# Optimization experiments

Hardware: AMD Instinct MI355X
Metric: run time of the kernel (lower is better)

## Reference

```python
import jax, jax.numpy as jnp
import numpy as np

B, S, D = 1, 2048, 2048
H = 16
HD = D // H           # 128
FFN_H = 5632          # int(2*4*D/3) rounded up to multiple of 256
EPS = 1e-5
ROPE_THETA = 10000.0


def rms_norm(x, w, eps=EPS):
    # x * rsqrt(mean(x^2, -1) + eps) * w
    return x * jax.lax.rsqrt(jnp.mean(x * x, axis=-1, keepdims=True) + eps) * w


def apply_rope(x, cos, sin):
    # x: [B, S, H, HD]; cos/sin: [S, HD//2]
    b, s, h, hd = x.shape
    xr = x.reshape(b, s, h, hd // 2, 2)
    x_re, x_im = xr[..., 0], xr[..., 1]
    c = cos[None, :, None, :]
    sn = sin[None, :, None, :]
    o_re = x_re * c - x_im * sn
    o_im = x_re * sn + x_im * c
    return jnp.stack([o_re, o_im], axis=-1).reshape(b, s, h, hd)


def setup_inputs() -> dict:
    key = jax.random.key(0)
    ks = jax.random.split(key, 10)
    x = jax.random.normal(ks[0], (B, S, D), dtype=jnp.float32)
    # RoPE frequencies (Llama-style)
    inv_freq = 1.0 / (ROPE_THETA ** (np.arange(0, HD, 2, dtype=np.float32) / HD))
    angles = np.outer(np.arange(S, dtype=np.float32), inv_freq)  # [S, HD//2]
    freqs_cos = jnp.asarray(np.cos(angles), dtype=jnp.float32)
    freqs_sin = jnp.asarray(np.sin(angles), dtype=jnp.float32)
    # causal mask: 1 = keep, 0 = masked
    mask = jnp.tril(jnp.ones((S, S), dtype=jnp.int32))[None, None]
    sc = 0.02
    return {
        "x": x,
        "freqs_cos": freqs_cos,
        "freqs_sin": freqs_sin,
        "mask": mask,
        "wq": jax.random.normal(ks[1], (D, D), jnp.float32) * sc,
        "wk": jax.random.normal(ks[2], (D, D), jnp.float32) * sc,
        "wv": jax.random.normal(ks[3], (D, D), jnp.float32) * sc,
        "wo": jax.random.normal(ks[4], (D, D), jnp.float32) * sc,
        "w1": jax.random.normal(ks[5], (D, FFN_H), jnp.float32) * sc,
        "w2": jax.random.normal(ks[6], (FFN_H, D), jnp.float32) * sc,
        "w3": jax.random.normal(ks[7], (D, FFN_H), jnp.float32) * sc,
        "attn_norm_w": jnp.ones((D,), jnp.float32),
        "ffn_norm_w": jnp.ones((D,), jnp.float32),
    }


def reference(x, freqs_cos, freqs_sin, mask, wq, wk, wv, wo, w1, w2, w3,
              attn_norm_w, ffn_norm_w):
    b, s, d = x.shape
    # --- attention block ---
    xn = rms_norm(x, attn_norm_w)
    q = (xn @ wq).reshape(b, s, H, HD)
    k = (xn @ wk).reshape(b, s, H, HD)
    v = (xn @ wv).reshape(b, s, H, HD)
    q = apply_rope(q, freqs_cos, freqs_sin)
    k = apply_rope(k, freqs_cos, freqs_sin)
    scores = jnp.einsum('bqhd,bkhd->bhqk', q, k) / jnp.sqrt(jnp.float32(HD))
    scores = jnp.where(mask == 0, -jnp.inf, scores)
    probs = jax.nn.softmax(scores, axis=-1)
    attn = jnp.einsum('bhqk,bkhd->bqhd', probs, v).reshape(b, s, d)
    h = x + attn @ wo
    # --- SwiGLU FFN block ---
    hn = rms_norm(h, ffn_norm_w)
    ff = (jax.nn.silu(hn @ w1) * (hn @ w3)) @ w2
    return h + ff
```

## Files before the change

kernel.cpp:

```cpp
#include <hip/hip_runtime.h>
#include <hip/hip_bf16.h>

typedef __bf16 bf16x8 __attribute__((ext_vector_type(8)));
typedef float f32x4 __attribute__((ext_vector_type(4)));
typedef unsigned short u16x8 __attribute__((ext_vector_type(8)));
typedef unsigned short u16x4 __attribute__((ext_vector_type(4)));

#define DEV static __device__ __forceinline__

DEV unsigned short f2bf(float f) {
    unsigned u = __builtin_bit_cast(unsigned, f);
    u += 0x7fffu + ((u >> 16) & 1u);
    return (unsigned short)(u >> 16);
}
DEV float bf2f(unsigned short h) {
    unsigned u = ((unsigned)h) << 16;
    return __builtin_bit_cast(float, u);
}

DEV void gl2lds16(const void* g, void* l) {
    __builtin_amdgcn_global_load_lds(
        (const __attribute__((address_space(1))) void*)g,
        (__attribute__((address_space(3))) void*)l, 16, 0, 0);
}

#define WAITV(N) asm volatile("s_waitcnt vmcnt(" #N ")" ::: "memory")
#define SBAR()   asm volatile("s_barrier" ::: "memory")

#define STAGE128D(KT, BUF)                                                    \
    _Pragma("unroll")                                                         \
    for (int sl = 0; sl < 3; ++sl) {                                          \
        const unsigned short* sbase = (sl == 0)                               \
            ? A  + (size_t)bm * K                                             \
            : BT + (size_t)(bn + (sl - 1) * 128) * K;                         \
        _Pragma("unroll")                                                     \
        for (int j = 0; j < 2; ++j) {                                         \
            const unsigned short* g = sbase + (size_t)(srow + j * 64) * K     \
                                      + koff + (KT) * 64 + lc;                \
            gl2lds16(g, &lds[BUF][sl][wave * 512 + j * 4096]);                \
        }                                                                     \
    }

#define DSREAD128(BUF)                                                        \
    {                                                                         \
        const char* Ab = (const char*)&lds[BUF][0][0];                        \
        const char* Bb = (const char*)&lds[BUF][1 + (wn >> 1)][0];            \
        _Pragma("unroll")                                                     \
        for (int m4 = 0; m4 < 4; ++m4)                                        \
            _Pragma("unroll")                                                 \
            for (int kk = 0; kk < 2; ++kk)                                    \
                a_[m4][kk] = *(const bf16x8*)(Ab +                            \
                    (wm * 64 + m4 * 16 + lr) * 128 +                          \
                    ((kk * 64 + lg * 16) ^ xsw));                             \
        _Pragma("unroll")                                                     \
        for (int n2 = 0; n2 < 4; ++n2)                                        \
            _Pragma("unroll")                                                 \
            for (int kk = 0; kk < 2; ++kk)                                    \
                b_[n2][kk] = *(const bf16x8*)(Bb +                            \
                    ((wn & 1) * 64 + n2 * 16 + lr) * 128 +                    \
                    ((kk * 64 + lg * 16) ^ xsw));                             \
    }

#define MFMA128                                                               \
    __builtin_amdgcn_s_setprio(1);                                            \
    _Pragma("unroll")                                                         \
    for (int m4 = 0; m4 < 4; ++m4)                                            \
        _Pragma("unroll")                                                     \
        for (int n2 = 0; n2 < 4; ++n2)                                        \
            _Pragma("unroll")                                                 \
            for (int kk = 0; kk < 2; ++kk)                                    \
                acc[m4][n2] = __builtin_amdgcn_mfma_f32_16x16x32_bf16(        \
                    a_[m4][kk], b_[n2][kk], acc[m4][n2], 0, 0, 0);            \
    __builtin_amdgcn_s_setprio(0);

template <int EPI>
__global__ __launch_bounds__(512, 2)
void gemm128d(const unsigned short* __restrict__ A,
              const unsigned short* __restrict__ BT,
              unsigned short* __restrict__ outB,
              float* __restrict__ outP,
              int M, int N, int K)
{
    __shared__ alignas(16) unsigned short lds[3][3][8192];
    const int tid  = threadIdx.x;
    const int lane = tid & 63;
    const int wave = tid >> 6;
    const int wm = wave >> 2;
    const int wn = wave & 3;
    const int lr = lane & 15;
    const int lg = lane >> 4;
    const int gy  = gridDim.y;
    const int lin = blockIdx.y * gridDim.x + blockIdx.x;
    const int cpx = (gridDim.x * gy) >> 3;
    const int swz = (lin & 7) * cpx + (lin >> 3);
    const int bm = (swz % gy) * 128;
    const int bn = (swz / gy) * 256;
    const int xsw  = (lr & 7) << 4;
    const int srow = tid >> 3;
    const int lc   = ((tid & 7) ^ (srow & 7)) * 8;
    int koff, NT;
    if constexpr (EPI == 1) { const int Kh = K >> 1; koff = blockIdx.z * Kh; NT = Kh >> 6; }
    else                    { koff = 0;              NT = K >> 6; }

    f32x4 acc[4][4] = {};
    bf16x8 a_[4][2], b_[4][2];

    STAGE128D(0, 0);
    STAGE128D(1, 1);
    WAITV(6); SBAR();
    DSREAD128(0);

    int bc = 0;
    for (int kt = 0; kt < NT - 2; ++kt) {
        const int nb = (bc == 0) ? 2 : bc - 1;
        STAGE128D(kt + 2, nb);
        MFMA128;
        WAITV(6); SBAR();
        const int rb = (bc == 2) ? 0 : bc + 1;
        DSREAD128(rb);
        bc = rb;
    }
    MFMA128;
    WAITV(0); SBAR();
    {
        const int rb = (bc == 2) ? 0 : bc + 1;
        DSREAD128(rb);
    }
    MFMA128;

#pragma unroll
    for (int m4 = 0; m4 < 4; ++m4) {
        const int row = bm + wm * 64 + m4 * 16 + lg * 4;
#pragma unroll
        for (int n2 = 0; n2 < 4; ++n2) {
            const int col = bn + wn * 64 + n2 * 16 + lr;
#pragma unroll
            for (int r = 0; r < 4; ++r) {
                if constexpr (EPI == 0) {
                    outB[(size_t)(row + r) * N + col] = f2bf(acc[m4][n2][r]);
                } else if constexpr (EPI == 1) {
                    outP[(size_t)blockIdx.z * M * N + (size_t)(row + r) * N + col] = acc[m4][n2][r];
                } else {
                    const float v  = acc[m4][n2][r];
                    const float vo = __shfl_xor(v, 1);
                    const float x1 = (lr & 1) ? vo : v;
                    const float x3 = (lr & 1) ? v : vo;
                    const float g  = x1 / (1.0f + __expf(-x1)) * x3;
                    if (!(lr & 1))
                        outB[(size_t)(row + r) * (N >> 1) + (col >> 1)] = f2bf(g);
                }
            }
        }
    }
}

__global__ __launch_bounds__(256)
void reduce2_add(const float* res, const float* p, float* out, int n4)
{
    const float4* r4 = (const float4*)res;
    const float4* a4 = (const float4*)p;
    const float4* b4 = (const float4*)(p + (size_t)2048 * 2048);
    float4* o4 = (float4*)out;
    for (int i = blockIdx.x * 256 + threadIdx.x; i < n4; i += gridDim.x * 256) {
        const float4 r = r4[i], a = a4[i], b = b4[i];
        o4[i] = make_float4(r.x + a.x + b.x, r.y + a.y + b.y,
                            r.z + a.z + b.z, r.w + a.w + b.w);
    }
}

__global__ __launch_bounds__(256)
void reduce2_norm(const float* __restrict__ res, const float* __restrict__ p,
                  const float* __restrict__ w, float* __restrict__ hout,
                  unsigned short* __restrict__ nout)
{
    const int row = blockIdx.x, tid = threadIdx.x;
    const float4* r4 = (const float4*)(res + (size_t)row * 2048);
    const float4* a4 = (const float4*)(p   + (size_t)row * 2048);
    const float4* b4 = (const float4*)(p + (size_t)2048 * 2048 + (size_t)row * 2048);
    float4* h4 = (float4*)(hout + (size_t)row * 2048);
    float4 h[2];
    float ss = 0.f;
#pragma unroll
    for (int i = 0; i < 2; ++i) {
        const int idx = i * 256 + tid;
        const float4 r = r4[idx], a = a4[idx], b = b4[idx];
        float4 v = make_float4(r.x + a.x + b.x, r.y + a.y + b.y,
                               r.z + a.z + b.z, r.w + a.w + b.w);
        h[i] = v; h4[idx] = v;
        ss += v.x * v.x + v.y * v.y + v.z * v.z + v.w * v.w;
    }
#pragma unroll
    for (int off = 32; off; off >>= 1) ss += __shfl_xor(ss, off);
    __shared__ float red[4];
    if ((tid & 63) == 0) red[tid >> 6] = ss;
    __syncthreads();
    const float tot = red[0] + red[1] + red[2] + red[3];
    const float sc = rsqrtf(tot * (1.0f / 2048.0f) + 1e-5f);
#pragma unroll
    for (int i = 0; i < 2; ++i) {
        const int idx = i * 256 + tid;
        const float4 wv = ((const float4*)w)[idx];
        u16x4 o;
        o[0] = f2bf(h[i].x * sc * wv.x); o[1] = f2bf(h[i].y * sc * wv.y);
        o[2] = f2bf(h[i].z * sc * wv.z); o[3] = f2bf(h[i].w * sc * wv.w);
        *(u16x4*)(nout + (size_t)row * 2048 + idx * 4) = o;
    }
}

__global__ __launch_bounds__(256)
void rmsnorm_kernel(const float* __restrict__ x, const float* __restrict__ w,
                    unsigned short* __restrict__ out)
{
    const int row = blockIdx.x;
    const int tid = threadIdx.x;
    const float* xr = x + (size_t)row * 2048;
    const float4 a = *reinterpret_cast<const float4*>(xr + tid * 8);
    const float4 b = *reinterpret_cast<const float4*>(xr + tid * 8 + 4);
    float ss = a.x * a.x + a.y * a.y + a.z * a.z + a.w * a.w
             + b.x * b.x + b.y * b.y + b.z * b.z + b.w * b.w;
#pragma unroll
    for (int off = 32; off; off >>= 1) ss += __shfl_xor(ss, off);
    __shared__ float red[4];
    if ((tid & 63) == 0) red[tid >> 6] = ss;
    __syncthreads();
    const float tot = red[0] + red[1] + red[2] + red[3];
    const float sc = rsqrtf(tot * (1.0f / 2048.0f) + 1e-5f);
    const float4 wa = *reinterpret_cast<const float4*>(w + tid * 8);
    const float4 wb = *reinterpret_cast<const float4*>(w + tid * 8 + 4);
    u16x8 o;
    o[0] = f2bf(a.x * sc * wa.x); o[1] = f2bf(a.y * sc * wa.y);
    o[2] = f2bf(a.z * sc * wa.z); o[3] = f2bf(a.w * sc * wa.w);
    o[4] = f2bf(b.x * sc * wb.x); o[5] = f2bf(b.y * sc * wb.y);
    o[6] = f2bf(b.z * sc * wb.z); o[7] = f2bf(b.w * sc * wb.w);
    *reinterpret_cast<u16x8*>(out + (size_t)row * 2048 + tid * 8) = o;
}

__global__ __launch_bounds__(256)
void rope_kernel(unsigned short* __restrict__ t, const float* __restrict__ cs,
                 const float* __restrict__ sn)
{
    const int idx = blockIdx.x * 256 + threadIdx.x;
    const int s   = idx >> 9;
    const int col = (idx & 511) * 8;
    const int i0  = (col & 127) >> 1;
    u16x8 v = *reinterpret_cast<const u16x8*>(t + (size_t)s * 6144 + col);
    const float4 c  = *reinterpret_cast<const float4*>(cs + s * 64 + i0);
    const float4 sv = *reinterpret_cast<const float4*>(sn + s * 64 + i0);
    const float cc[4] = {c.x, c.y, c.z, c.w};
    const float ns[4] = {sv.x, sv.y, sv.z, sv.w};
#pragma unroll
    for (int p = 0; p < 4; ++p) {
        const float re = bf2f(v[2 * p]), im = bf2f(v[2 * p + 1]);
        v[2 * p]     = f2bf(re * cc[p] - im * ns[p]);
        v[2 * p + 1] = f2bf(re * ns[p] + im * cc[p]);
    }
    *reinterpret_cast<u16x8*>(t + (size_t)s * 6144 + col) = v;
}

__global__ __launch_bounds__(256)
void transpose_bf16(const unsigned short* __restrict__ in,
                    unsigned short* __restrict__ out, int M, int N, int ldin)
{
    __shared__ unsigned short t[64][66];
    const int bm = blockIdx.y * 64, bn = blockIdx.x * 64;
    const int tid = threadIdx.x;
    const int r = tid >> 3, c8 = (tid & 7) * 8;
#pragma unroll
    for (int i = 0; i < 2; ++i) {
        const int row = r + i * 32;
        u16x8 v = *reinterpret_cast<const u16x8*>(in + (size_t)(bm + row) * ldin + bn + c8);
#pragma unroll
        for (int e = 0; e < 8; ++e) t[row][c8 + e] = v[e];
    }
    __syncthreads();
#pragma unroll
    for (int i = 0; i < 2; ++i) {
        const int orow = r + i * 32;
        u16x8 v;
#pragma unroll
        for (int e = 0; e < 8; ++e) v[e] = t[c8 + e][orow];
        *reinterpret_cast<u16x8*>(out + (size_t)(bn + orow) * M + bm + c8) = v;
    }
}

__global__ __launch_bounds__(256)
void convT_kernel(const float* __restrict__ w, unsigned short* __restrict__ wT,
                  int K, int N, int rmul, int radd)
{
    __shared__ unsigned short t[64][66];
    const int bk = blockIdx.y * 64, bn = blockIdx.x * 64;
    const int tid = threadIdx.x;
    const int r = tid >> 4, c4 = (tid & 15) * 4;
#pragma unroll
    for (int i = 0; i < 4; ++i) {
        const int row = r + i * 16;
        const float4 v = *reinterpret_cast<const float4*>(w + (size_t)(bk + row) * N + bn + c4);
        t[row][c4 + 0] = f2bf(v.x); t[row][c4 + 1] = f2bf(v.y);
        t[row][c4 + 2] = f2bf(v.z); t[row][c4 + 3] = f2bf(v.w);
    }
    __syncthreads();
#pragma unroll
    for (int i = 0; i < 4; ++i) {
        const int n = r + i * 16;
        u16x4 o;
#pragma unroll
        for (int e = 0; e < 4; ++e) o[e] = t[c4 + e][n];
        *reinterpret_cast<u16x4*>(wT + (size_t)(rmul * (bn + n) + radd) * K + bk + c4) = o;
    }
}

__global__ __launch_bounds__(512)
void flash_attn(const unsigned short* __restrict__ q,
                const unsigned short* __restrict__ k,
                const unsigned short* __restrict__ vT,
                unsigned short* __restrict__ attn)
{
    __shared__ alignas(16) unsigned short Ks[2][64][136];
    __shared__ alignas(16) unsigned short Vs[2][128][72];
    __shared__ alignas(16) unsigned short Ps[8][16][72];

    const int hh = blockIdx.y;
    const int pi = blockIdx.x;
    const int tid = threadIdx.x;
    const int lane = tid & 63, wave = tid >> 6;
    const int qt = (wave >> 2) ? (31 - pi) : pi;
    const int lr = lane & 15, lg = lane >> 4;
    const int q0 = qt * 64 + (wave & 3) * 16;
    const int myNT = qt + 1;
    const int NT   = 32 - pi;

    const int kr0 = tid >> 4, kc0 = (tid & 15) * 8;
    const int vr0 = tid >> 3, vc0 = (tid & 7) * 8;

    bf16x8 qf[4];
#pragma unroll
    for (int c = 0; c < 4; ++c)
        qf[c] = *reinterpret_cast<const bf16x8*>(
            q + (size_t)(q0 + lr) * 6144 + hh * 128 + c * 32 + lg * 8);

    f32x4 oacc[8] = {};
    float m_r[4], l_r[4];
#pragma unroll
    for (int r = 0; r < 4; ++r) { m_r[r] = -INFINITY; l_r[r] = 0.0f; }
    const float scale = 0.08838834764831845f;

    u16x8 kreg0, kreg1, vreg0, vreg1;
    auto gload = [&](int kt) {
        const int kv0 = kt * 64;
        kreg0 = *reinterpret_cast<const u16x8*>(k + (size_t)(kv0 + kr0) * 6144 + hh * 128 + kc0);
        kreg1 = *reinterpret_cast<const u16x8*>(k + (size_t)(kv0 + kr0 + 32) * 6144 + hh * 128 + kc0);
        vreg0 = *reinterpret_cast<const u16x8*>(vT + (size_t)(hh * 128 + vr0) * 2048 + kv0 + vc0);
        vreg1 = *reinterpret_cast<const u16x8*>(vT + (size_t)(hh * 128 + vr0 + 64) * 2048 + kv0 + vc0);
    };
    auto lwrite = [&](int buf) {
        *reinterpret_cast<u16x8*>(&Ks[buf][kr0][kc0])      = kreg0;
        *reinterpret_cast<u16x8*>(&Ks[buf][kr0 + 32][kc0]) = kreg1;
        *reinterpret_cast<u16x8*>(&Vs[buf][vr0][vc0])      = vreg0;
        *reinterpret_cast<u16x8*>(&Vs[buf][vr0 + 64][vc0]) = vreg1;
    };

    gload(0); lwrite(0);
    __syncthreads();

    for (int kt = 0; kt < NT; ++kt) {
        const int buf = kt & 1;
        if (kt + 1 < NT) gload(kt + 1);

        if (kt < myNT) {
            const int kv0 = kt * 64;
            const bool masked = (kt == myNT - 1);
            f32x4 s[4] = {};
            __builtin_amdgcn_s_setprio(1);
#pragma unroll
            for (int ct = 0; ct < 4; ++ct)
#pragma unroll
                for (int c = 0; c < 4; ++c) {
                    const bf16x8 kf = *reinterpret_cast<const bf16x8*>(
                        &Ks[buf][ct * 16 + lr][c * 32 + lg * 8]);
                    s[ct] = __builtin_amdgcn_mfma_f32_16x16x32_bf16(qf[c], kf, s[ct], 0, 0, 0);
                }
            __builtin_amdgcn_s_setprio(0);
#pragma unroll
            for (int ct = 0; ct < 4; ++ct)
#pragma unroll
                for (int r = 0; r < 4; ++r) {
                    float v = s[ct][r] * scale;
                    if (masked) {
                        const int kvg = kv0 + ct * 16 + lr;
                        const int qg  = q0 + lg * 4 + r;
                        if (kvg > qg) v = -INFINITY;
                    }
                    s[ct][r] = v;
                }
            float mn[4], alpha[4], rs[4];
#pragma unroll
            for (int r = 0; r < 4; ++r) {
                float v = fmaxf(fmaxf(s[0][r], s[1][r]), fmaxf(s[2][r], s[3][r]));
                v = fmaxf(v, __shfl_xor(v, 1));
                v = fmaxf(v, __shfl_xor(v, 2));
                v = fmaxf(v, __shfl_xor(v, 4));
                v = fmaxf(v, __shfl_xor(v, 8));
                mn[r] = fmaxf(m_r[r], v);
                alpha[r] = __expf(m_r[r] - mn[r]);
                m_r[r] = mn[r];
                rs[r] = 0.0f;
            }
#pragma unroll
            for (int ct = 0; ct < 4; ++ct)
#pragma unroll
                for (int r = 0; r < 4; ++r) {
                    const float p = __expf(s[ct][r] - mn[r]);
                    s[ct][r] = p;
                    rs[r] += p;
                }
#pragma unroll
            for (int r = 0; r < 4; ++r) {
                float t2 = rs[r];
                t2 += __shfl_xor(t2, 1);
                t2 += __shfl_xor(t2, 2);
                t2 += __shfl_xor(t2, 4);
                t2 += __shfl_xor(t2, 8);
                l_r[r] = l_r[r] * alpha[r] + t2;
            }
#pragma unroll
            for (int ot = 0; ot < 8; ++ot)
#pragma unroll
                for (int r = 0; r < 4; ++r) oacc[ot][r] *= alpha[r];

#pragma unroll
            for (int ct = 0; ct < 4; ++ct)
#pragma unroll
                for (int r = 0; r < 4; ++r)
                    Ps[wave][lg * 4 + r][ct * 16 + lr] = f2bf(s[ct][r]);

            __builtin_amdgcn_s_setprio(1);
#pragma unroll
            for (int c2 = 0; c2 < 2; ++c2) {
                const bf16x8 pf = *reinterpret_cast<const bf16x8*>(
                    &Ps[wave][lr][c2 * 32 + lg * 8]);
#pragma unroll
                for (int ot = 0; ot < 8; ++ot) {
                    const bf16x8 vf = *reinterpret_cast<const bf16x8*>(
                        &Vs[buf][ot * 16 + lr][c2 * 32 + lg * 8]);
                    oacc[ot] = __builtin_amdgcn_mfma_f32_16x16x32_bf16(pf, vf, oacc[ot], 0, 0, 0);
                }
            }
            __builtin_amdgcn_s_setprio(0);
        }

        if (kt + 1 < NT) lwrite(buf ^ 1);
        __syncthreads();
    }

#pragma unroll
    for (int ot = 0; ot < 8; ++ot)
#pragma unroll
        for (int r = 0; r < 4; ++r) {
            const float v = oacc[ot][r] / l_r[r];
            attn[(size_t)(q0 + lg * 4 + r) * 2048 + hh * 128 + ot * 16 + lr] = f2bf(v);
        }
}

extern "C" void kernel_launch(void* const* d_in, const int* in_sizes, int n_in,
                              void* d_out, int out_size, void* d_ws, size_t ws_size,
                              hipStream_t stream)
{
    const float* x    = (const float*)d_in[0];
    const float* fcos = (const float*)d_in[1];
    const float* fsin = (const float*)d_in[2];
    const float* wq  = (const float*)d_in[4];
    const float* wk  = (const float*)d_in[5];
    const float* wv  = (const float*)d_in[6];
    const float* wo  = (const float*)d_in[7];
    const float* w1  = (const float*)d_in[8];
    const float* w2  = (const float*)d_in[9];
    const float* w3  = (const float*)d_in[10];
    const float* anw = (const float*)d_in[11];
    const float* fnw = (const float*)d_in[12];
    float* out = (float*)d_out;

    char* ws = (char*)d_ws;
    size_t off = 0;
    auto alloc = [&](size_t bytes) { void* p = ws + off; off += bytes; return p; };
    const size_t SZ_DD = (size_t)2048 * 2048 * 2;
    const size_t SZ_DF = (size_t)2048 * 5632 * 2;

    unsigned short* wqT  = (unsigned short*)alloc(SZ_DD);
    unsigned short* wkT  = (unsigned short*)alloc(SZ_DD);
    unsigned short* wvT  = (unsigned short*)alloc(SZ_DD);
    unsigned short* woT  = (unsigned short*)alloc(SZ_DD);
    unsigned short* w13T = (unsigned short*)alloc(2 * SZ_DF);
    unsigned short* w2T  = (unsigned short*)alloc(SZ_DF);

    char* reg1 = (char*)alloc((size_t)48 * 1024 * 1024);
    unsigned short* xn   = (unsigned short*)reg1;
    unsigned short* qkv  = (unsigned short*)(reg1 + SZ_DD);
    unsigned short* vTb  = (unsigned short*)(reg1 + SZ_DD + 3 * SZ_DD);
    unsigned short* ab   = (unsigned short*)(reg1 + SZ_DD + 4 * SZ_DD);
    float*          pk   = (float*)reg1;
    unsigned short* hn   = (unsigned short*)(reg1 + 4 * SZ_DD);

    char* reg2 = (char*)alloc(SZ_DF);
    unsigned short* t1 = (unsigned short*)reg2;

    const int N4 = 2048 * 2048 / 4;

    convT_kernel<<<dim3(32, 32), 256, 0, stream>>>(wq, wqT, 2048, 2048, 1, 0);
    convT_kernel<<<dim3(32, 32), 256, 0, stream>>>(wk, wkT, 2048, 2048, 1, 0);
    convT_kernel<<<dim3(32, 32), 256, 0, stream>>>(wv, wvT, 2048, 2048, 1, 0);
    convT_kernel<<<dim3(32, 32), 256, 0, stream>>>(wo, woT, 2048, 2048, 1, 0);
    convT_kernel<<<dim3(88, 32), 256, 0, stream>>>(w1, w13T, 2048, 5632, 2, 0);
    convT_kernel<<<dim3(88, 32), 256, 0, stream>>>(w3, w13T, 2048, 5632, 2, 1);
    convT_kernel<<<dim3(32, 88), 256, 0, stream>>>(w2, w2T, 5632, 2048, 1, 0);

    rmsnorm_kernel<<<2048, 256, 0, stream>>>(x, anw, xn);
    gemm128d<0><<<dim3(24, 16), 512, 0, stream>>>(xn, wqT, qkv, nullptr, 2048, 6144, 2048);
    rope_kernel<<<4096, 256, 0, stream>>>(qkv, fcos, fsin);
    transpose_bf16<<<dim3(32, 32), 256, 0, stream>>>(qkv + 4096, vTb, 2048, 2048, 6144);
    flash_attn<<<dim3(16, 16), 512, 0, stream>>>(qkv, qkv + 2048, vTb, ab);
    gemm128d<1><<<dim3(8, 16, 2), 512, 0, stream>>>(ab, woT, nullptr, pk, 2048, 2048, 2048);
    reduce2_norm<<<2048, 256, 0, stream>>>(x, pk, fnw, out, hn);

    gemm128d<2><<<dim3(44, 16), 512, 0, stream>>>(hn, w13T, t1, nullptr, 2048, 11264, 2048);
    gemm128d<1><<<dim3(8, 16, 2), 512, 0, stream>>>(t1, w2T, nullptr, pk, 2048, 2048, 5632);
    reduce2_add<<<2048, 256, 0, stream>>>(out, pk, out, N4);
}
```

Before: 434.7 us.

## Fuse RoPE and V-transpose into QKV GEMM, atomic-add split-K, batch weight conversion

Several changes land together. RoPE and the V transpose move into the QKV GEMM epilogue, so the separate rope and transpose kernels go away. The final FFN split-K GEMM atomically adds its partials into the output, which removes the reduce2_add pass. The seven weight-conversion launches become three batched launches. The GEMM main loop also splits its LDS reads per k-half so the second read overlaps the first set of MFMAs. The costs are scattered cos/sin loads and uncoalesced 4-element vT stores in the epilogue, plus non-deterministic float atomics.

```diff
diff --git a/kernel.cpp b/kernel.cpp
--- a/kernel.cpp
+++ b/kernel.cpp
@@ -41,36 +41,30 @@
         }                                                                     \
     }
 
-#define DSREAD128(BUF)                                                        \
+#define DSREAD_K(BUF, KK, AR, BR)                                             \
     {                                                                         \
         const char* Ab = (const char*)&lds[BUF][0][0];                        \
         const char* Bb = (const char*)&lds[BUF][1 + (wn >> 1)][0];            \
         _Pragma("unroll")                                                     \
         for (int m4 = 0; m4 < 4; ++m4)                                        \
-            _Pragma("unroll")                                                 \
-            for (int kk = 0; kk < 2; ++kk)                                    \
-                a_[m4][kk] = *(const bf16x8*)(Ab +                            \
-                    (wm * 64 + m4 * 16 + lr) * 128 +                          \
-                    ((kk * 64 + lg * 16) ^ xsw));                             \
+            AR[m4] = *(const bf16x8*)(Ab +                                    \
+                (wm * 64 + m4 * 16 + lr) * 128 +                              \
+                (((KK) * 64 + lg * 16) ^ xsw));                               \
         _Pragma("unroll")                                                     \
         for (int n2 = 0; n2 < 4; ++n2)                                        \
-            _Pragma("unroll")                                                 \
-            for (int kk = 0; kk < 2; ++kk)                                    \
-                b_[n2][kk] = *(const bf16x8*)(Bb +                            \
-                    ((wn & 1) * 64 + n2 * 16 + lr) * 128 +                    \
-                    ((kk * 64 + lg * 16) ^ xsw));                             \
-    }
-
-#define MFMA128                                                               \
+            BR[n2] = *(const bf16x8*)(Bb +                                    \
+                ((wn & 1) * 64 + n2 * 16 + lr) * 128 +                        \
+                (((KK) * 64 + lg * 16) ^ xsw));                               \
+    }
+
+#define MFMA16(AR, BR)                                                        \
     __builtin_amdgcn_s_setprio(1);                                            \
     _Pragma("unroll")                                                         \
     for (int m4 = 0; m4 < 4; ++m4)                                            \
         _Pragma("unroll")                                                     \
         for (int n2 = 0; n2 < 4; ++n2)                                        \
-            _Pragma("unroll")                                                 \
-            for (int kk = 0; kk < 2; ++kk)                                    \
-                acc[m4][n2] = __builtin_amdgcn_mfma_f32_16x16x32_bf16(        \
-                    a_[m4][kk], b_[n2][kk], acc[m4][n2], 0, 0, 0);            \
+            acc[m4][n2] = __builtin_amdgcn_mfma_f32_16x16x32_bf16(            \
+                AR[m4], BR[n2], acc[m4][n2], 0, 0, 0);                        \
     __builtin_amdgcn_s_setprio(0);
 
 template <int EPI>
@@ -79,7 +73,9 @@
               const unsigned short* __restrict__ BT,
               unsigned short* __restrict__ outB,
               float* __restrict__ outP,
-              int M, int N, int K)
+              int M, int N, int K,
+              const float* __restrict__ cs, const float* __restrict__ sn,
+              unsigned short* __restrict__ vT)
 {
     __shared__ alignas(16) unsigned short lds[3][3][8192];
     const int tid  = threadIdx.x;
@@ -99,34 +95,44 @@
     const int srow = tid >> 3;
     const int lc   = ((tid & 7) ^ (srow & 7)) * 8;
     int koff, NT;
-    if constexpr (EPI == 1) { const int Kh = K >> 1; koff = blockIdx.z * Kh; NT = Kh >> 6; }
-    else                    { koff = 0;              NT = K >> 6; }
+    if constexpr (EPI == 1 || EPI == 3) {
+        const int Kh = K >> 1; koff = blockIdx.z * Kh; NT = Kh >> 6;
+    } else {
+        koff = 0; NT = K >> 6;
+    }
 
     f32x4 acc[4][4] = {};
-    bf16x8 a_[4][2], b_[4][2];
+    bf16x8 a0[4], b0[4], a1[4], b1[4];
 
     STAGE128D(0, 0);
     STAGE128D(1, 1);
     WAITV(6); SBAR();
-    DSREAD128(0);
+    DSREAD_K(0, 0, a0, b0);
 
     int bc = 0;
     for (int kt = 0; kt < NT - 2; ++kt) {
         const int nb = (bc == 0) ? 2 : bc - 1;
         STAGE128D(kt + 2, nb);
-        MFMA128;
+        MFMA16(a0, b0);
+        DSREAD_K(bc, 1, a1, b1);
+        MFMA16(a1, b1);
         WAITV(6); SBAR();
         const int rb = (bc == 2) ? 0 : bc + 1;
-        DSREAD128(rb);
+        DSREAD_K(rb, 0, a0, b0);
         bc = rb;
     }
-    MFMA128;
+    MFMA16(a0, b0);
+    DSREAD_K(bc, 1, a1, b1);
+    MFMA16(a1, b1);
     WAITV(0); SBAR();
     {
         const int rb = (bc == 2) ? 0 : bc + 1;
-        DSREAD128(rb);
-    }
-    MFMA128;
+        DSREAD_K(rb, 0, a0, b0);
+        bc = rb;
+    }
+    MFMA16(a0, b0);
+    DSREAD_K(bc, 1, a1, b1);
+    MFMA16(a1, b1);
 
 #pragma unroll
     for (int m4 = 0; m4 < 4; ++m4) {
@@ -134,37 +140,47 @@
 #pragma unroll
         for (int n2 = 0; n2 < 4; ++n2) {
             const int col = bn + wn * 64 + n2 * 16 + lr;
-#pragma unroll
-            for (int r = 0; r < 4; ++r) {
-                if constexpr (EPI == 0) {
-                    outB[(size_t)(row + r) * N + col] = f2bf(acc[m4][n2][r]);
-                } else if constexpr (EPI == 1) {
-                    outP[(size_t)blockIdx.z * M * N + (size_t)(row + r) * N + col] = acc[m4][n2][r];
+            if constexpr (EPI == 4) {
+                if (bn >= 4096) {
+                    u16x4 o;
+#pragma unroll
+                    for (int r = 0; r < 4; ++r) o[r] = f2bf(acc[m4][n2][r]);
+                    *(u16x4*)(vT + (size_t)(col - 4096) * 2048 + row) = o;
                 } else {
-                    const float v  = acc[m4][n2][r];
-                    const float vo = __shfl_xor(v, 1);
-                    const float x1 = (lr & 1) ? vo : v;
-                    const float x3 = (lr & 1) ? v : vo;
-                    const float g  = x1 / (1.0f + __expf(-x1)) * x3;
-                    if (!(lr & 1))
-                        outB[(size_t)(row + r) * (N >> 1) + (col >> 1)] = f2bf(g);
+#pragma unroll
+                    for (int r = 0; r < 4; ++r) {
+                        const float v  = acc[m4][n2][r];
+                        const float vo = __shfl_xor(v, 1);
+                        const int rr = row + r;
+                        const int i0 = (col & 127) >> 1;
+                        const float c = cs[rr * 64 + i0];
+                        const float s = sn[rr * 64 + i0];
+                        const float o = (lr & 1) ? (vo * s + v * c)
+                                                 : (v * c - vo * s);
+                        outB[(size_t)rr * N + col] = f2bf(o);
+                    }
+                }
+            } else {
+#pragma unroll
+                for (int r = 0; r < 4; ++r) {
+                    if constexpr (EPI == 0) {
+                        outB[(size_t)(row + r) * N + col] = f2bf(acc[m4][n2][r]);
+                    } else if constexpr (EPI == 1) {
+                        outP[(size_t)blockIdx.z * M * N + (size_t)(row + r) * N + col] = acc[m4][n2][r];
+                    } else if constexpr (EPI == 3) {
+                        unsafeAtomicAdd(&outP[(size_t)(row + r) * N + col], acc[m4][n2][r]);
+                    } else {
+                        const float v  = acc[m4][n2][r];
+                        const float vo = __shfl_xor(v, 1);
+                        const float x1 = (lr & 1) ? vo : v;
+                        const float x3 = (lr & 1) ? v : vo;
+                        const float g  = x1 / (1.0f + __expf(-x1)) * x3;
+                        if (!(lr & 1))
+                            outB[(size_t)(row + r) * (N >> 1) + (col >> 1)] = f2bf(g);
+                    }
                 }
             }
         }
-    }
-}
-
-__global__ __launch_bounds__(256)
-void reduce2_add(const float* res, const float* p, float* out, int n4)
-{
-    const float4* r4 = (const float4*)res;
-    const float4* a4 = (const float4*)p;
-    const float4* b4 = (const float4*)(p + (size_t)2048 * 2048);
-    float4* o4 = (float4*)out;
-    for (int i = blockIdx.x * 256 + threadIdx.x; i < n4; i += gridDim.x * 256) {
-        const float4 r = r4[i], a = a4[i], b = b4[i];
-        o4[i] = make_float4(r.x + a.x + b.x, r.y + a.y + b.y,
-                            r.z + a.z + b.z, r.w + a.w + b.w);
     }
 }
 
@@ -235,61 +251,10 @@
     *reinterpret_cast<u16x8*>(out + (size_t)row * 2048 + tid * 8) = o;
 }
 
-__global__ __launch_bounds__(256)
-void rope_kernel(unsigned short* __restrict__ t, const float* __restrict__ cs,
-                 const float* __restrict__ sn)
-{
-    const int idx = blockIdx.x * 256 + threadIdx.x;
-    const int s   = idx >> 9;
-    const int col = (idx & 511) * 8;
-    const int i0  = (col & 127) >> 1;
-    u16x8 v = *reinterpret_cast<const u16x8*>(t + (size_t)s * 6144 + col);
-    const float4 c  = *reinterpret_cast<const float4*>(cs + s * 64 + i0);
-    const float4 sv = *reinterpret_cast<const float4*>(sn + s * 64 + i0);
-    const float cc[4] = {c.x, c.y, c.z, c.w};
-    const float ns[4] = {sv.x, sv.y, sv.z, sv.w};
-#pragma unroll
-    for (int p = 0; p < 4; ++p) {
-        const float re = bf2f(v[2 * p]), im = bf2f(v[2 * p + 1]);
-        v[2 * p]     = f2bf(re * cc[p] - im * ns[p]);
-        v[2 * p + 1] = f2bf(re * ns[p] + im * cc[p]);
-    }
-    *reinterpret_cast<u16x8*>(t + (size_t)s * 6144 + col) = v;
-}
-
-__global__ __launch_bounds__(256)
-void transpose_bf16(const unsigned short* __restrict__ in,
-                    unsigned short* __restrict__ out, int M, int N, int ldin)
+DEV void convT_body(const float* __restrict__ w, unsigned short* __restrict__ wT,
+                    int K, int N, int rmul, int radd, int bk, int bn, int tid)
 {
     __shared__ unsigned short t[64][66];
-    const int bm = blockIdx.y * 64, bn = blockIdx.x * 64;
-    const int tid = threadIdx.x;
-    const int r = tid >> 3, c8 = (tid & 7) * 8;
-#pragma unroll
-    for (int i = 0; i < 2; ++i) {
-        const int row = r + i * 32;
-        u16x8 v = *reinterpret_cast<const u16x8*>(in + (size_t)(bm + row) * ldin + bn + c8);
-#pragma unroll
-        for (int e = 0; e < 8; ++e) t[row][c8 + e] = v[e];
-    }
-    __syncthreads();
-#pragma unroll
-    for (int i = 0; i < 2; ++i) {
-        const int orow = r + i * 32;
-        u16x8 v;
-#pragma unroll
-        for (int e = 0; e < 8; ++e) v[e] = t[c8 + e][orow];
-        *reinterpret_cast<u16x8*>(out + (size_t)(bn + orow) * M + bm + c8) = v;
-    }
-}
-
-__global__ __launch_bounds__(256)
-void convT_kernel(const float* __restrict__ w, unsigned short* __restrict__ wT,
-                  int K, int N, int rmul, int radd)
-{
-    __shared__ unsigned short t[64][66];
-    const int bk = blockIdx.y * 64, bn = blockIdx.x * 64;
-    const int tid = threadIdx.x;
     const int r = tid >> 4, c4 = (tid & 15) * 4;
 #pragma unroll
     for (int i = 0; i < 4; ++i) {
@@ -307,6 +272,33 @@
         for (int e = 0; e < 4; ++e) o[e] = t[c4 + e][n];
         *reinterpret_cast<u16x4*>(wT + (size_t)(rmul * (bn + n) + radd) * K + bk + c4) = o;
     }
+}
+
+__global__ __launch_bounds__(256)
+void convT_kernel(const float* __restrict__ w, unsigned short* __restrict__ wT,
+                  int K, int N)
+{
+    convT_body(w, wT, K, N, 1, 0, blockIdx.y * 64, blockIdx.x * 64, threadIdx.x);
+}
+
+__global__ __launch_bounds__(256)
+void convT4_kernel(const float* __restrict__ w0, const float* __restrict__ w1,
+                   const float* __restrict__ w2, const float* __restrict__ w3,
+                   unsigned short* __restrict__ wT)
+{
+    const int z = blockIdx.z;
+    const float* w = (z == 0) ? w0 : (z == 1) ? w1 : (z == 2) ? w2 : w3;
+    convT_body(w, wT + (size_t)z * 2048 * 2048, 2048, 2048, 1, 0,
+               blockIdx.y * 64, blockIdx.x * 64, threadIdx.x);
+}
+
+__global__ __launch_bounds__(256)
+void convTpair_kernel(const float* __restrict__ wa, const float* __restrict__ wb,
+                      unsigned short* __restrict__ wT)
+{
+    const int z = blockIdx.z;
+    convT_body(z ? wb : wa, wT, 2048, 5632, 2, z,
+               blockIdx.y * 64, blockIdx.x * 64, threadIdx.x);
 }
 
 __global__ __launch_bounds__(512)
@@ -485,12 +477,9 @@
     const size_t SZ_DD = (size_t)2048 * 2048 * 2;
     const size_t SZ_DF = (size_t)2048 * 5632 * 2;
 
-    unsigned short* wqT  = (unsigned short*)alloc(SZ_DD);
-    unsigned short* wkT  = (unsigned short*)alloc(SZ_DD);
-    unsigned short* wvT  = (unsigned short*)alloc(SZ_DD);
-    unsigned short* woT  = (unsigned short*)alloc(SZ_DD);
-    unsigned short* w13T = (unsigned short*)alloc(2 * SZ_DF);
-    unsigned short* w2T  = (unsigned short*)alloc(SZ_DF);
+    unsigned short* qkvoT = (unsigned short*)alloc(4 * SZ_DD);
+    unsigned short* w13T  = (unsigned short*)alloc(2 * SZ_DF);
+    unsigned short* w2T   = (unsigned short*)alloc(SZ_DF);
 
     char* reg1 = (char*)alloc((size_t)48 * 1024 * 1024);
     unsigned short* xn   = (unsigned short*)reg1;
@@ -503,25 +492,23 @@
     char* reg2 = (char*)alloc(SZ_DF);
     unsigned short* t1 = (unsigned short*)reg2;
 
-    const int N4 = 2048 * 2048 / 4;
-
-    convT_kernel<<<dim3(32, 32), 256, 0, stream>>>(wq, wqT, 2048, 2048, 1, 0);
-    convT_kernel<<<dim3(32, 32), 256, 0, stream>>>(wk, wkT, 2048, 2048, 1, 0);
-    convT_kernel<<<dim3(32, 32), 256, 0, stream>>>(wv, wvT, 2048, 2048, 1, 0);
-    convT_kernel<<<dim3(32, 32), 256, 0, stream>>>(wo, woT, 2048, 2048, 1, 0);
-    convT_kernel<<<dim3(88, 32), 256, 0, stream>>>(w1, w13T, 2048, 5632, 2, 0);
-    convT_kernel<<<dim3(88, 32), 256, 0, stream>>>(w3, w13T, 2048, 5632, 2, 1);
-    convT_kernel<<<dim3(32, 88), 256, 0, stream>>>(w2, w2T, 5632, 2048, 1, 0);
+    convT4_kernel<<<dim3(32, 32, 4), 256, 0, stream>>>(wq, wk, wv, wo, qkvoT);
+    convTpair_kernel<<<dim3(88, 32, 2), 256, 0, stream>>>(w1, w3, w13T);
+    convT_kernel<<<dim3(32, 88), 256, 0, stream>>>(w2, w2T, 5632, 2048);
 
     rmsnorm_kernel<<<2048, 256, 0, stream>>>(x, anw, xn);
-    gemm128d<0><<<dim3(24, 16), 512, 0, stream>>>(xn, wqT, qkv, nullptr, 2048, 6144, 2048);
-    rope_kernel<<<4096, 256, 0, stream>>>(qkv, fcos, fsin);
-    transpose_bf16<<<dim3(32, 32), 256, 0, stream>>>(qkv + 4096, vTb, 2048, 2048, 6144);
+    gemm128d<4><<<dim3(24, 16), 512, 0, stream>>>(xn, qkvoT, qkv, nullptr,
+                                                  2048, 6144, 2048, fcos, fsin, vTb);
     flash_attn<<<dim3(16, 16), 512, 0, stream>>>(qkv, qkv + 2048, vTb, ab);
-    gemm128d<1><<<dim3(8, 16, 2), 512, 0, stream>>>(ab, woT, nullptr, pk, 2048, 2048, 2048);
+    gemm128d<1><<<dim3(8, 16, 2), 512, 0, stream>>>(ab, qkvoT + 3 * (size_t)2048 * 2048,
+                                                    nullptr, pk, 2048, 2048, 2048,
+                                                    nullptr, nullptr, nullptr);
     reduce2_norm<<<2048, 256, 0, stream>>>(x, pk, fnw, out, hn);
 
-    gemm128d<2><<<dim3(44, 16), 512, 0, stream>>>(hn, w13T, t1, nullptr, 2048, 11264, 2048);
-    gemm128d<1><<<dim3(8, 16, 2), 512, 0, stream>>>(t1, w2T, nullptr, pk, 2048, 2048, 5632);
-    reduce2_add<<<2048, 256, 0, stream>>>(out, pk, out, N4);
-}
+    gemm128d<2><<<dim3(44, 16), 512, 0, stream>>>(hn, w13T, t1, nullptr,
+                                                  2048, 11264, 2048,
+                                                  nullptr, nullptr, nullptr);
+    gemm128d<3><<<dim3(8, 16, 2), 512, 0, stream>>>(t1, w2T, nullptr, out,
+                                                    2048, 2048, 5632,
+                                                    nullptr, nullptr, nullptr);
+}
```

Measured after the change: 438.0 us. About the same (+0.8%).
